# Performance work log

Hardware: AMD Instinct MI355X
Metric: run time of the kernel (lower is better)

## Reference

```python
import jax, jax.numpy as jnp
import numpy as np

B, T, W = 4, 2048, 1024
K, G = 7, 8            # kernel_size, groups
Cg = W // G            # channels per group
SE_R = 16              # SE reduction ratio
LN_EPS = 1e-5


def setup_inputs() -> dict:
    key = jax.random.key(0)
    ks = jax.random.split(key, 8)
    h = jax.random.normal(ks[0], (B, T, W), jnp.float32)
    # mask: True = padding; valid prefix of random length per row
    lengths = jax.random.randint(ks[1], (B,), T // 2, T + 1)
    mask = jnp.arange(T)[None, :] >= lengths[:, None]
    s_w = np.float32(1.0 / np.sqrt(W))
    return dict(
        h=h,
        mask=mask,
        offset_w=jax.random.normal(ks[2], (W, K), jnp.float32) * 0.01,
        offset_b=jnp.zeros((K,), jnp.float32),
        conv_w=jax.random.normal(ks[3], (G, Cg, Cg, K), jnp.float32) * np.float32(1.0 / np.sqrt(Cg * K)),
        conv_b=jnp.zeros((W,), jnp.float32),
        ln_g=jnp.ones((W,), jnp.float32),
        ln_b=jnp.zeros((W,), jnp.float32),
        se_w1=jax.random.normal(ks[4], (W, W // SE_R), jnp.float32) * s_w,
        se_b1=jnp.zeros((W // SE_R,), jnp.float32),
        se_w2=jax.random.normal(ks[5], (W // SE_R, W), jnp.float32) * np.float32(1.0 / np.sqrt(W // SE_R)),
        se_b2=jnp.zeros((W,), jnp.float32),
        proj_w=jax.random.normal(ks[6], (W, 1), jnp.float32) * s_w,
        proj_b=jnp.zeros((1,), jnp.float32),
    )


def deform_conv1d(h, offset_w, offset_b, conv_w, conv_b):
    # h: [B,T,W]. Learned per-(position, tap) fractional offsets; linear interp gather;
    # grouped conv combine. conv_w: [G, out_per_group, in_per_group, K].
    Bn, Tn, Wn = h.shape
    pad = (K - 1) // 2
    offsets = h @ offset_w + offset_b                                   # [B,T,K]
    base = (jnp.arange(Tn, dtype=jnp.float32)[None, :, None]
            + (jnp.arange(K, dtype=jnp.float32) - pad)[None, None, :])  # [1,T,K]
    pos = jnp.clip(base + offsets, 0.0, Tn - 1.0)                       # [B,T,K]
    p0 = jnp.floor(pos).astype(jnp.int32)
    p1 = jnp.minimum(p0 + 1, Tn - 1)
    frac = (pos - p0.astype(jnp.float32))[..., None]                    # [B,T,K,1]
    gather = jax.vmap(lambda hb, ib: hb[ib])                            # [T,W],[T,K] -> [T,K,W]
    sampled = gather(h, p0) * (1.0 - frac) + gather(h, p1) * frac       # [B,T,K,W]
    sg = sampled.reshape(Bn, Tn, K, G, Cg)
    out = jnp.einsum('btkgc,gock->btgo', sg, conv_w).reshape(Bn, Tn, Wn)
    return out + conv_b


def layer_norm(x, g, b):
    mu = jnp.mean(x, axis=-1, keepdims=True)
    var = jnp.mean(jnp.square(x - mu), axis=-1, keepdims=True)
    return (x - mu) * jax.lax.rsqrt(var + LN_EPS) * g + b


def se_block(x, mask, w1, b1, w2, b2):
    valid = (~mask).astype(x.dtype)[..., None]                          # [B,T,1]
    lengths = jnp.clip(jnp.sum(valid, axis=1), 1.0)                     # [B,1]
    s = jnp.sum(x * valid, axis=1) / lengths                            # [B,W]
    gate = jax.nn.sigmoid(jax.nn.relu(s @ w1 + b1) @ w2 + b2)           # [B,W]
    return x * gate[:, None, :]


def reference(h, mask, offset_w, offset_b, conv_w, conv_b, ln_g, ln_b,
              se_w1, se_b1, se_w2, se_b2, proj_w, proj_b):
    x = layer_norm(deform_conv1d(h, offset_w, offset_b, conv_w, conv_b), ln_g, ln_b)
    x = se_block(x, mask, se_w1, se_b1, se_w2, se_b2)
    # dropout: identity in eval mode (p handled outside reference)
    valid = (~mask).astype(x.dtype)[..., None]
    x = x * valid                                                       # masked_fill(mask, 0)
    lengths = jnp.clip(jnp.sum(valid, axis=1), 1.0)                     # [B,1]
    pooled = jnp.sum(x, axis=1) / lengths                               # [B,W]
    return jnp.squeeze(pooled @ proj_w + proj_b, axis=-1)               # [B]
```

## Files before the change

### kernel.cpp

```cpp
#include <hip/hip_runtime.h>
#include <hip/hip_bf16.h>

#define Bdim 4
#define Tdim 2048
#define Wdim 1024
#define Kdim 7
#define Gdim 8
#define Cg   128
#define Hdim 64
#define TT   64

typedef __attribute__((ext_vector_type(8))) short short8v;
typedef __attribute__((ext_vector_type(4))) float float4v;

__device__ __forceinline__ short f2bf(float x) {
    union { float f; unsigned u; } v; v.f = x;
    unsigned r = v.u + 0x7fff + ((v.u >> 16) & 1);
    return (short)(r >> 16);
}

__device__ __forceinline__ unsigned pack2bf(float lo, float hi) {
    return __builtin_amdgcn_perm(__float_as_uint(hi) + 0x8000u,
                                 __float_as_uint(lo) + 0x8000u, 0x07060302u);
}

__device__ __forceinline__ short8v lerp_pack(uint4 a, uint4 b, float f) {
    union { uint4 u; short8v s; } r;
    const unsigned* pa = (const unsigned*)&a;
    const unsigned* pb = (const unsigned*)&b;
    unsigned* pr = (unsigned*)&r.u;
#pragma unroll
    for (int d = 0; d < 4; d++) {
        float alo = __uint_as_float(pa[d] << 16);
        float ahi = __uint_as_float(pa[d] & 0xffff0000u);
        float blo = __uint_as_float(pb[d] << 16);
        float bhi = __uint_as_float(pb[d] & 0xffff0000u);
        float rlo = alo + f * (blo - alo);
        float rhi = ahi + f * (bhi - ahi);
        pr[d] = pack2bf(rlo, rhi);
    }
    return r.s;
}

__global__ __launch_bounds__(256) void k_pre(const float* __restrict__ conv_w,
                                             short* __restrict__ Wtb,
                                             const float* __restrict__ h,
                                             const float* __restrict__ offset_w,
                                             const float* __restrict__ offset_b,
                                             float* __restrict__ pos,
                                             ushort* __restrict__ h16,
                                             float* __restrict__ rowstat) {
    int tid = threadIdx.x;
    if (blockIdx.x < 448) {
        if (blockIdx.x < 64) rowstat[blockIdx.x * 256 + tid] = 0.f;
        int i = blockIdx.x * 256 + tid;
        int cb = i & 15;
        int o = (i >> 4) & 127;
        int gk = i >> 11;
        int k = gk % Kdim, g = gk / Kdim;
        const float* src = conv_w + ((size_t)(g * Cg + o) * Cg + cb * 8) * Kdim + k;
        short8v pk;
#pragma unroll
        for (int j = 0; j < 8; j++) pk[j] = f2bf(src[(size_t)j * Kdim]);
        short8v* Wtb8 = (short8v*)Wtb;
        Wtb8[(size_t)gk * 2048 + o * 16 + cb] = pk;
        return;
    }
    int lane = tid & 63, wv = tid >> 6;
    int bt = (blockIdx.x - 448) * 4 + wv;
    int t = bt & (Tdim - 1);
    const float* row = h + (size_t)bt * Wdim;
    float acc[Kdim];
#pragma unroll
    for (int k = 0; k < Kdim; k++) acc[k] = 0.f;
#pragma unroll
    for (int j = 0; j < 4; j++) {
        int c = lane * 4 + j * 256;
        float4 hv = *(const float4*)(row + c);
        const float* ow = offset_w + (size_t)c * Kdim;
#pragma unroll
        for (int k = 0; k < Kdim; k++)
            acc[k] += hv.x * ow[k] + hv.y * ow[Kdim + k] + hv.z * ow[2 * Kdim + k]
                    + hv.w * ow[3 * Kdim + k];
        ushort4 hp;
        hp.x = (ushort)f2bf(hv.x); hp.y = (ushort)f2bf(hv.y);
        hp.z = (ushort)f2bf(hv.z); hp.w = (ushort)f2bf(hv.w);
        *(ushort4*)(h16 + (size_t)bt * Wdim + c) = hp;
    }
#pragma unroll
    for (int k = 0; k < Kdim; k++) {
#pragma unroll
        for (int m = 32; m > 0; m >>= 1) acc[k] += __shfl_xor(acc[k], m);
    }
    if (lane < Kdim) {
        float o = acc[lane] + offset_b[lane];
        float base = (float)t + (float)(lane - 3);
        float p = fminf(fmaxf(base + o, 0.f), (float)(Tdim - 1));
        pos[bt * Kdim + lane] = p;
    }
}

__global__ __launch_bounds__(256, 3) void k_conv(const ushort* __restrict__ h16,
                                                 const short* __restrict__ Wtb,
                                                 const float* __restrict__ conv_b,
                                                 const float* __restrict__ pos,
                                                 ushort* __restrict__ y16,
                                                 float* __restrict__ rowstat) {
    __shared__ short8v sA8[2][TT * 16];
    __shared__ float posl[TT * 8];

    int blk = blockIdx.x;
    int g  = blk & 7;
    int tc = (blk >> 3) & 31;
    int b  = blk >> 8;
    int t0 = tc * TT;
    int tid = threadIdx.x;
    int lane = tid & 63, wv = tid >> 6;
    int r15 = lane & 15, q = lane >> 4;

    const ushort* hb = h16 + (size_t)(b * Tdim) * Wdim + g * Cg;
    const short8v* WtbV = (const short8v*)Wtb + (size_t)(g * Kdim) * 2048;

    int scb = tid & 15;
    int sr0 = tid >> 4;

    {
        int base = (b * Tdim + t0) * Kdim;
        for (int u = tid; u < TT * Kdim; u += 256) {
            int r = u / 7, kk = u - r * 7;
            posl[r * 8 + kk] = pos[base + u];
        }
    }
    __syncthreads();

    float4v acc[4][2];
#pragma unroll
    for (int tt = 0; tt < 4; tt++)
#pragma unroll
        for (int n = 0; n < 2; n++) acc[tt][n] = (float4v){0.f, 0.f, 0.f, 0.f};

    float fr[4];
    uint4 glo[4], ghi[4];
    short8v bfr[8];
#pragma unroll
    for (int i = 0; i < 4; i++) {
        int r = sr0 + i * 16;
        float p = posl[r * 8 + 0];
        int p0 = (int)p;
        fr[i] = p - (float)p0;
        int p1 = min(p0 + 1, Tdim - 1);
        glo[i] = *(const uint4*)(hb + (size_t)p0 * Wdim + scb * 8);
        ghi[i] = *(const uint4*)(hb + (size_t)p1 * Wdim + scb * 8);
    }
#pragma unroll
    for (int n = 0; n < 2; n++)
#pragma unroll
        for (int kk = 0; kk < 4; kk++)
            bfr[n * 4 + kk] = WtbV[(wv * 32 + n * 16 + r15) * 16 + kk * 4 + q];

#pragma unroll 1
    for (int k = 0; k < Kdim; k++) {
        short8v* buf = sA8[k & 1];
#pragma unroll
        for (int i = 0; i < 4; i++) {
            int r = sr0 + i * 16;
            buf[r * 16 + (scb ^ (r & 7))] = lerp_pack(glo[i], ghi[i], fr[i]);
        }
        __syncthreads();
        if (k < Kdim - 1) {
#pragma unroll
            for (int i = 0; i < 4; i++) {
                int r = sr0 + i * 16;
                float p = posl[r * 8 + k + 1];
                int p0 = (int)p;
                fr[i] = p - (float)p0;
                int p1 = min(p0 + 1, Tdim - 1);
                glo[i] = *(const uint4*)(hb + (size_t)p0 * Wdim + scb * 8);
                ghi[i] = *(const uint4*)(hb + (size_t)p1 * Wdim + scb * 8);
            }
        }
        __builtin_amdgcn_sched_barrier(0);
#pragma unroll
        for (int tt = 0; tt < 4; tt++) {
            int r = tt * 16 + r15;
            short8v af[4];
#pragma unroll
            for (int kk = 0; kk < 4; kk++)
                af[kk] = buf[r * 16 + ((kk * 4 + q) ^ (r & 7))];
#pragma unroll
            for (int kk = 0; kk < 4; kk++) {
#pragma unroll
                for (int n = 0; n < 2; n++)
                    acc[tt][n] = __builtin_amdgcn_mfma_f32_16x16x32_bf16(
                        af[kk], bfr[n * 4 + kk], acc[tt][n], 0, 0, 0);
            }
        }
        __builtin_amdgcn_sched_barrier(0);
        if (k < Kdim - 1) {
#pragma unroll
            for (int n = 0; n < 2; n++)
#pragma unroll
                for (int kk = 0; kk < 4; kk++)
                    bfr[n * 4 + kk] =
                        WtbV[(size_t)(k + 1) * 2048 + (wv * 32 + n * 16 + r15) * 16 + kk * 4 + q];
        }
    }
    __syncthreads();
    float* ep = (float*)sA8;
#pragma unroll
    for (int n = 0; n < 2; n++) {
        int colb = wv * 32 + n * 16 + r15;
        float bias = conv_b[g * Cg + colb];
#pragma unroll
        for (int tt = 0; tt < 4; tt++)
#pragma unroll
            for (int j = 0; j < 4; j++) {
                int row = tt * 16 + q * 4 + j;
                ep[row * 128 + (colb ^ ((row & 7) << 2))] = acc[tt][n][j] + bias;
            }
    }
    __syncthreads();
    int row = tid >> 2, c0 = (tid & 3) * 32;
    int sw = (row & 7) << 2;
    ushort* yp = y16 + (size_t)(b * Tdim + t0 + row) * Wdim + g * Cg + c0;
    float s_part = 0.f, q_part = 0.f;
#pragma unroll
    for (int s = 0; s < 4; s++) {
        float4 va = *(const float4*)&ep[row * 128 + ((c0 + s * 8) ^ sw)];
        float4 vb = *(const float4*)&ep[row * 128 + ((c0 + s * 8 + 4) ^ sw)];
        s_part += va.x + va.y + va.z + va.w + vb.x + vb.y + vb.z + vb.w;
        q_part += va.x * va.x + va.y * va.y + va.z * va.z + va.w * va.w
                + vb.x * vb.x + vb.y * vb.y + vb.z * vb.z + vb.w * vb.w;
        uint4 o;
        o.x = pack2bf(va.x, va.y);
        o.y = pack2bf(va.z, va.w);
        o.z = pack2bf(vb.x, vb.y);
        o.w = pack2bf(vb.z, vb.w);
        *(uint4*)(yp + s * 8) = o;
    }
    s_part += __shfl_xor(s_part, 1); s_part += __shfl_xor(s_part, 2);
    q_part += __shfl_xor(q_part, 1); q_part += __shfl_xor(q_part, 2);
    if ((tid & 3) == 0) {
        atomicAdd(&rowstat[(b * Tdim + t0 + row) * 2 + 0], s_part);
        atomicAdd(&rowstat[(b * Tdim + t0 + row) * 2 + 1], q_part);
    }
}

__global__ __launch_bounds__(256) void k_lnpool(const ushort* __restrict__ y16,
                                                const int* __restrict__ mask,
                                                const float* __restrict__ rowstat,
                                                float* __restrict__ part) {
    int blk = blockIdx.x;
    int b = blk >> 6, ch = blk & 63;
    int tid = threadIdx.x;
    int c0 = tid * 4;
    float a0 = 0.f, a1 = 0.f, a2 = 0.f, a3 = 0.f;
    for (int i = 0; i < 32; i++) {
        int t = ch * 32 + i;
        if (mask[b * Tdim + t]) continue;
        float2 st = *(const float2*)(rowstat + (b * Tdim + t) * 2);
        float mu = st.x * (1.f / Wdim);
        float inv = rsqrtf(st.y * (1.f / Wdim) - mu * mu + 1e-5f);
        uint2 u = *(const uint2*)(y16 + (size_t)(b * Tdim + t) * Wdim + c0);
        float v0 = __uint_as_float(u.x << 16);
        float v1 = __uint_as_float(u.x & 0xffff0000u);
        float v2 = __uint_as_float(u.y << 16);
        float v3 = __uint_as_float(u.y & 0xffff0000u);
        a0 += (v0 - mu) * inv; a1 += (v1 - mu) * inv;
        a2 += (v2 - mu) * inv; a3 += (v3 - mu) * inv;
    }
    *(float4*)(part + (size_t)blk * Wdim + c0) = (float4){a0, a1, a2, a3};
}

__global__ __launch_bounds__(256) void k_sefinal(const float* __restrict__ part,
                                                 const int* __restrict__ mask,
                                                 const float* __restrict__ ln_g,
                                                 const float* __restrict__ ln_b,
                                                 const float* __restrict__ w1,
                                                 const float* __restrict__ b1,
                                                 const float* __restrict__ w2,
                                                 const float* __restrict__ b2,
                                                 const float* __restrict__ projw,
                                                 const float* __restrict__ projb,
                                                 float* __restrict__ out) {
    int b = blockIdx.x, tid = threadIdx.x;
    __shared__ float s[Wdim];
    __shared__ float hred[4][Hdim];
    __shared__ float hid[Hdim];
    __shared__ float rbuf[4];
    __shared__ float sLinv;
    int lane = tid & 63, wv = tid >> 6;

    int cnt = 0;
    for (int t = tid; t < Tdim; t += 256) cnt += (mask[b * Tdim + t] ? 0 : 1);
    float fc = (float)cnt;
#pragma unroll
    for (int off = 32; off > 0; off >>= 1) fc += __shfl_down(fc, off);
    if (lane == 0) rbuf[wv] = fc;
    __syncthreads();
    if (tid == 0) {
        float L = rbuf[0] + rbuf[1] + rbuf[2] + rbuf[3];
        sLinv = 1.f / fmaxf(L, 1.f);
    }
    __syncthreads();
    float Linv = sLinv;

    int w4 = tid * 4;
    float4 a = {0.f, 0.f, 0.f, 0.f};
    for (int chh = 0; chh < 64; chh++) {
        float4 p = *(const float4*)(part + (size_t)(b * 64 + chh) * Wdim + w4);
        a.x += p.x; a.y += p.y; a.z += p.z; a.w += p.w;
    }
    float4 gg = *(const float4*)(ln_g + w4);
    float4 bb = *(const float4*)(ln_b + w4);
    s[w4 + 0] = gg.x * (a.x * Linv) + bb.x;
    s[w4 + 1] = gg.y * (a.y * Linv) + bb.y;
    s[w4 + 2] = gg.z * (a.z * Linv) + bb.z;
    s[w4 + 3] = gg.w * (a.w * Linv) + bb.w;
    __syncthreads();

    int j = tid & 63, p = tid >> 6;
    float ha = 0.f;
    for (int w = p * 256; w < (p + 1) * 256; ++w) ha += s[w] * w1[(size_t)w * Hdim + j];
    hred[p][j] = ha;
    __syncthreads();
    if (tid < Hdim)
        hid[tid] = fmaxf(hred[0][tid] + hred[1][tid] + hred[2][tid] + hred[3][tid] + b1[tid], 0.f);
    __syncthreads();

    float part2 = 0.f;
    for (int w = tid; w < Wdim; w += 256) {
        float ga = b2[w];
#pragma unroll 8
        for (int j2 = 0; j2 < Hdim; j2++) ga += hid[j2] * w2[(size_t)j2 * Wdim + w];
        float gate = 1.f / (1.f + expf(-ga));
        part2 += s[w] * gate * projw[w];
    }
#pragma unroll
    for (int off = 32; off > 0; off >>= 1) part2 += __shfl_down(part2, off);
    __syncthreads();
    if (lane == 0) rbuf[wv] = part2;
    __syncthreads();
    if (tid == 0) out[b] = rbuf[0] + rbuf[1] + rbuf[2] + rbuf[3] + projb[0];
}

extern "C" void kernel_launch(void* const* d_in, const int* in_sizes, int n_in,
                              void* d_out, int out_size, void* d_ws, size_t ws_size,
                              hipStream_t stream) {
    const float* h        = (const float*)d_in[0];
    const int*   mask     = (const int*)d_in[1];
    const float* offset_w = (const float*)d_in[2];
    const float* offset_b = (const float*)d_in[3];
    const float* conv_w   = (const float*)d_in[4];
    const float* conv_b   = (const float*)d_in[5];
    const float* ln_g     = (const float*)d_in[6];
    const float* ln_b     = (const float*)d_in[7];
    const float* se_w1    = (const float*)d_in[8];
    const float* se_b1    = (const float*)d_in[9];
    const float* se_w2    = (const float*)d_in[10];
    const float* se_b2    = (const float*)d_in[11];
    const float* proj_w   = (const float*)d_in[12];
    const float* proj_b   = (const float*)d_in[13];
    float* out = (float*)d_out;

    char* wsb = (char*)d_ws;
    float*  pos     = (float*)(wsb);
    ushort* h16     = (ushort*)(wsb + 229376);
    short*  Wtb     = (short*)(wsb + 17006592);
    ushort* y16     = (ushort*)(wsb + 18841600);
    float*  rowstat = (float*)(wsb + 35618816);
    float*  part    = (float*)(wsb + 35684352);

    k_pre<<<dim3(448 + Bdim * Tdim / 4), dim3(256), 0, stream>>>(conv_w, Wtb, h, offset_w,
                                                                 offset_b, pos, h16, rowstat);
    k_conv<<<dim3(Bdim * (Tdim / TT) * Gdim), dim3(256), 0, stream>>>(h16, Wtb, conv_b,
                                                                      pos, y16, rowstat);
    k_lnpool<<<dim3(Bdim * 64), dim3(256), 0, stream>>>(y16, mask, rowstat, part);
    k_sefinal<<<dim3(Bdim), dim3(256), 0, stream>>>(part, mask, ln_g, ln_b,
                                                    se_w1, se_b1, se_w2, se_b2,
                                                    proj_w, proj_b, out);
}
```

Measured before the change: 105.8 us.

## Stage offset weights in LDS, raise conv occupancy, reload B fragments per tap

```diff
diff --git a/kernel.cpp b/kernel.cpp
--- a/kernel.cpp
+++ b/kernel.cpp
@@ -66,41 +66,54 @@
         Wtb8[(size_t)gk * 2048 + o * 16 + cb] = pk;
         return;
     }
+    __shared__ float ow_t[Kdim * Wdim];
     int lane = tid & 63, wv = tid >> 6;
-    int bt = (blockIdx.x - 448) * 4 + wv;
-    int t = bt & (Tdim - 1);
-    const float* row = h + (size_t)bt * Wdim;
-    float acc[Kdim];
-#pragma unroll
-    for (int k = 0; k < Kdim; k++) acc[k] = 0.f;
-#pragma unroll
-    for (int j = 0; j < 4; j++) {
-        int c = lane * 4 + j * 256;
-        float4 hv = *(const float4*)(row + c);
-        const float* ow = offset_w + (size_t)c * Kdim;
-#pragma unroll
-        for (int k = 0; k < Kdim; k++)
-            acc[k] += hv.x * ow[k] + hv.y * ow[Kdim + k] + hv.z * ow[2 * Kdim + k]
-                    + hv.w * ow[3 * Kdim + k];
-        ushort4 hp;
-        hp.x = (ushort)f2bf(hv.x); hp.y = (ushort)f2bf(hv.y);
-        hp.z = (ushort)f2bf(hv.z); hp.w = (ushort)f2bf(hv.w);
-        *(ushort4*)(h16 + (size_t)bt * Wdim + c) = hp;
-    }
-#pragma unroll
-    for (int k = 0; k < Kdim; k++) {
-#pragma unroll
-        for (int m = 32; m > 0; m >>= 1) acc[k] += __shfl_xor(acc[k], m);
-    }
-    if (lane < Kdim) {
-        float o = acc[lane] + offset_b[lane];
-        float base = (float)t + (float)(lane - 3);
-        float p = fminf(fmaxf(base + o, 0.f), (float)(Tdim - 1));
-        pos[bt * Kdim + lane] = p;
-    }
-}
-
-__global__ __launch_bounds__(256, 3) void k_conv(const ushort* __restrict__ h16,
+    for (int u = tid; u < Kdim * Wdim; u += 256) {
+        int c = u / Kdim, k = u - c * Kdim;
+        ow_t[k * Wdim + c] = offset_w[u];
+    }
+    __syncthreads();
+    int base = (blockIdx.x - 448) * 16 + wv * 4;
+#pragma unroll 1
+    for (int i = 0; i < 4; i++) {
+        int bt = base + i;
+        int t = bt & (Tdim - 1);
+        const float* hrow = h + (size_t)bt * Wdim;
+        float acc[Kdim];
+#pragma unroll
+        for (int k = 0; k < Kdim; k++) acc[k] = 0.f;
+#pragma unroll
+        for (int j = 0; j < 4; j++) {
+            int c = lane * 4 + j * 256;
+            float4 hv = *(const float4*)(hrow + c);
+#pragma unroll
+            for (int k = 0; k < Kdim; k++) {
+                float4 wk = *(const float4*)&ow_t[k * Wdim + c];
+                acc[k] += hv.x * wk.x + hv.y * wk.y + hv.z * wk.z + hv.w * wk.w;
+            }
+            ushort4 hp;
+            hp.x = (ushort)f2bf(hv.x); hp.y = (ushort)f2bf(hv.y);
+            hp.z = (ushort)f2bf(hv.z); hp.w = (ushort)f2bf(hv.w);
+            *(ushort4*)(h16 + (size_t)bt * Wdim + c) = hp;
+        }
+#pragma unroll
+        for (int k = 0; k < Kdim; k++) {
+#pragma unroll
+            for (int m = 32; m > 0; m >>= 1) acc[k] += __shfl_xor(acc[k], m);
+        }
+        if (lane == 0) {
+#pragma unroll
+            for (int k = 0; k < Kdim; k++) {
+                float o = acc[k] + offset_b[k];
+                float bs = (float)t + (float)(k - 3);
+                float p = fminf(fmaxf(bs + o, 0.f), (float)(Tdim - 1));
+                pos[bt * Kdim + k] = p;
+            }
+        }
+    }
+}
+
+__global__ __launch_bounds__(256, 4) void k_conv(const ushort* __restrict__ h16,
                                                  const short* __restrict__ Wtb,
                                                  const float* __restrict__ conv_b,
                                                  const float* __restrict__ pos,
@@ -141,7 +154,6 @@
 
     float fr[4];
     uint4 glo[4], ghi[4];
-    short8v bfr[8];
 #pragma unroll
     for (int i = 0; i < 4; i++) {
         int r = sr0 + i * 16;
@@ -152,14 +164,16 @@
         glo[i] = *(const uint4*)(hb + (size_t)p0 * Wdim + scb * 8);
         ghi[i] = *(const uint4*)(hb + (size_t)p1 * Wdim + scb * 8);
     }
-#pragma unroll
-    for (int n = 0; n < 2; n++)
-#pragma unroll
-        for (int kk = 0; kk < 4; kk++)
-            bfr[n * 4 + kk] = WtbV[(wv * 32 + n * 16 + r15) * 16 + kk * 4 + q];
 
 #pragma unroll 1
     for (int k = 0; k < Kdim; k++) {
+        short8v bfr[8];
+#pragma unroll
+        for (int n = 0; n < 2; n++)
+#pragma unroll
+            for (int kk = 0; kk < 4; kk++)
+                bfr[n * 4 + kk] =
+                    WtbV[(size_t)k * 2048 + (wv * 32 + n * 16 + r15) * 16 + kk * 4 + q];
         short8v* buf = sA8[k & 1];
 #pragma unroll
         for (int i = 0; i < 4; i++) {
@@ -179,7 +193,6 @@
                 ghi[i] = *(const uint4*)(hb + (size_t)p1 * Wdim + scb * 8);
             }
         }
-        __builtin_amdgcn_sched_barrier(0);
 #pragma unroll
         for (int tt = 0; tt < 4; tt++) {
             int r = tt * 16 + r15;
@@ -194,15 +207,6 @@
                     acc[tt][n] = __builtin_amdgcn_mfma_f32_16x16x32_bf16(
                         af[kk], bfr[n * 4 + kk], acc[tt][n], 0, 0, 0);
             }
-        }
-        __builtin_amdgcn_sched_barrier(0);
-        if (k < Kdim - 1) {
-#pragma unroll
-            for (int n = 0; n < 2; n++)
-#pragma unroll
-                for (int kk = 0; kk < 4; kk++)
-                    bfr[n * 4 + kk] =
-                        WtbV[(size_t)(k + 1) * 2048 + (wv * 32 + n * 16 + r15) * 16 + kk * 4 + q];
         }
     }
     __syncthreads();
@@ -255,6 +259,7 @@
     int tid = threadIdx.x;
     int c0 = tid * 4;
     float a0 = 0.f, a1 = 0.f, a2 = 0.f, a3 = 0.f;
+#pragma unroll 4
     for (int i = 0; i < 32; i++) {
         int t = ch * 32 + i;
         if (mask[b * Tdim + t]) continue;
@@ -371,8 +376,8 @@
     float*  rowstat = (float*)(wsb + 35618816);
     float*  part    = (float*)(wsb + 35684352);
 
-    k_pre<<<dim3(448 + Bdim * Tdim / 4), dim3(256), 0, stream>>>(conv_w, Wtb, h, offset_w,
-                                                                 offset_b, pos, h16, rowstat);
+    k_pre<<<dim3(448 + 512), dim3(256), 0, stream>>>(conv_w, Wtb, h, offset_w,
+                                                     offset_b, pos, h16, rowstat);
     k_conv<<<dim3(Bdim * (Tdim / TT) * Gdim), dim3(256), 0, stream>>>(h16, Wtb, conv_b,
                                                                       pos, y16, rowstat);
     k_lnpool<<<dim3(Bdim * 64), dim3(256), 0, stream>>>(y16, mask, rowstat, part);
```

Result: faster. 102.0 us, median of 2 (-3.6%).
